# Kernel tuning notes

Measured on AMD Instinct MI355X. Metric: run time of the kernel, lower is better.

The kernel has to match this reference:

```python
import jax, jax.numpy as jnp
import numpy as np

B, N = 8192, 512
WEIGHT_THRESHOLD = 0.0
EPS = 1e-5


def setup_inputs() -> dict:
    key = jax.random.key(0)
    k1, k2, k3 = jax.random.split(key, 3)
    src_points = jax.random.normal(k1, (B, N, 3), dtype=jnp.float32)
    tgt_points = jax.random.normal(k2, (B, N, 3), dtype=jnp.float32)
    weights = jax.random.uniform(k3, (B, N), dtype=jnp.float32)
    return {"src_points": src_points, "tgt_points": tgt_points, "weights": weights}


def _weighted_procrustes(src, tgt, w):
    # threshold + normalize weights  (B, N)
    w = jnp.where(w < WEIGHT_THRESHOLD, jnp.zeros_like(w), w)
    w = w / (jnp.sum(w, axis=1, keepdims=True) + EPS)
    w3 = w[..., None]                                   # (B, N, 1)
    # weighted centroids (B, 1, 3)
    src_c = jnp.sum(w3 * src, axis=1, keepdims=True)
    tgt_c = jnp.sum(w3 * tgt, axis=1, keepdims=True)
    src0 = src - src_c
    tgt0 = tgt - tgt_c
    # weighted covariance H = src0^T (w * tgt0)  -> (B, 3, 3)
    H = jnp.einsum("bni,bnj->bij", src0, w3 * tgt0)
    U, S, Vh = jnp.linalg.svd(H)
    V = jnp.swapaxes(Vh, -1, -2)
    Ut = jnp.swapaxes(U, -1, -2)
    # reflection correction: diag(1, 1, sign(det(V U^T)))
    det = jnp.linalg.det(jnp.matmul(V, Ut))             # (B,)
    ones = jnp.ones((src.shape[0], 2), dtype=src.dtype)
    d = jnp.concatenate([ones, jnp.sign(det)[:, None]], axis=1)  # (B, 3)
    R = jnp.einsum("bij,bj,bjk->bik", V, d, Ut)         # (B, 3, 3)
    t = tgt_c[:, 0, :] - jnp.einsum("bij,bj->bi", R, src_c[:, 0, :])  # (B, 3)
    return R, t


def reference(src_points, tgt_points, weights):
    return _weighted_procrustes(src_points, tgt_points, weights)
```

## Files before the change

kernel.cpp:

```cpp
#include <hip/hip_runtime.h>

#define NPTS 512
#define BLOCK 256
#define XPS 68

__global__ __launch_bounds__(BLOCK) void wproc_moments(
    const float* __restrict__ src,
    const float* __restrict__ tgt,
    const float* __restrict__ wts,
    float* __restrict__ ws)
{
    const int b = blockIdx.x;
    const int t = threadIdx.x;
    const int wave = t >> 6, lane = t & 63;

    __shared__ float s_s[NPTS * 3];
    __shared__ float s_t[NPTS * 3];
    __shared__ float xp[4][16][XPS];
    __shared__ float red[4][16];

    {
        const float4* sb4 = (const float4*)(src + (size_t)b * (NPTS * 3));
        const float4* tb4 = (const float4*)(tgt + (size_t)b * (NPTS * 3));
        float4* ss4 = (float4*)s_s;
        float4* st4 = (float4*)s_t;
        ss4[t] = sb4[t];
        st4[t] = tb4[t];
        if (t < 128) { ss4[256 + t] = sb4[256 + t]; st4[256 + t] = tb4[256 + t]; }
    }
    const float* wb = wts + (size_t)b * NPTS;
    float wA = wb[t];
    float wB = wb[t + 256];
    __syncthreads();

    float acc[16];
    #pragma unroll
    for (int i = 0; i < 16; ++i) acc[i] = 0.f;

    #pragma unroll
    for (int k = 0; k < 2; ++k) {
        const int p = t + k * 256;
        float w = k ? wB : wA;
        w = (w < 0.f) ? 0.f : w;
        const float sx = s_s[3 * p + 0], sy = s_s[3 * p + 1], sz = s_s[3 * p + 2];
        const float tx = s_t[3 * p + 0], ty = s_t[3 * p + 1], tz = s_t[3 * p + 2];
        acc[0] += w;
        acc[1] += w * sx; acc[2] += w * sy; acc[3] += w * sz;
        acc[4] += w * tx; acc[5] += w * ty; acc[6] += w * tz;
        const float wsx = w * sx, wsy = w * sy, wsz = w * sz;
        acc[7]  += wsx * tx; acc[8]  += wsx * ty; acc[9]  += wsx * tz;
        acc[10] += wsy * tx; acc[11] += wsy * ty; acc[12] += wsy * tz;
        acc[13] += wsz * tx; acc[14] += wsz * ty; acc[15] += wsz * tz;
    }

    #pragma unroll
    for (int m = 0; m < 16; ++m) xp[wave][m][lane] = acc[m];
    __syncthreads();

    {
        const int m = lane & 15, q = lane >> 4;
        const float4* row = (const float4*)&xp[wave][m][0] + 4 * q;
        float4 a0 = row[0], a1 = row[1], a2 = row[2], a3 = row[3];
        a0.x += a1.x; a0.y += a1.y; a0.z += a1.z; a0.w += a1.w;
        a2.x += a3.x; a2.y += a3.y; a2.z += a3.z; a2.w += a3.w;
        a0.x += a2.x; a0.y += a2.y; a0.z += a2.z; a0.w += a2.w;
        float v = (a0.x + a0.y) + (a0.z + a0.w);
        v += __shfl_xor(v, 16, 64);
        v += __shfl_xor(v, 32, 64);
        if (q == 0) red[wave][m] = v;
    }
    __syncthreads();

    if (t < 16) {
        ws[(size_t)b * 16 + t] =
            (red[0][t] + red[1][t]) + (red[2][t] + red[3][t]);
    }
}

__global__ __launch_bounds__(BLOCK) void wproc_solve(
    const float* __restrict__ ws,
    float* __restrict__ out,
    int B)
{
    const int b = blockIdx.x * BLOCK + threadIdx.x;
    if (b >= B) return;

    double m[16];
    #pragma unroll
    for (int i = 0; i < 16; ++i) m[i] = (double)ws[(size_t)b * 16 + i];

    const double T = m[0] + 1e-5;
    const double f = 2.0 - m[0] / T;
    const double cs[3] = { m[1] / T, m[2] / T, m[3] / T };
    const double ct[3] = { m[4] / T, m[5] / T, m[6] / T };
    double H[3][3];
    for (int i = 0; i < 3; ++i)
        for (int j = 0; j < 3; ++j)
            H[i][j] = m[7 + i * 3 + j] / T - f * cs[i] * ct[j];

    double A[3][3];
    for (int i = 0; i < 3; ++i)
        for (int j = 0; j < 3; ++j)
            A[i][j] = H[0][i] * H[0][j] + H[1][i] * H[1][j] + H[2][i] * H[2][j];

    double V[3][3] = { {1, 0, 0}, {0, 1, 0}, {0, 0, 1} };
    for (int sweep = 0; sweep < 5; ++sweep) {
        for (int pair = 0; pair < 3; ++pair) {
            const int p = (pair == 2) ? 1 : 0;
            const int q = (pair == 0) ? 1 : 2;
            const double apq = A[p][q];
            if (apq == 0.0) continue;
            const double theta = (A[q][q] - A[p][p]) / (2.0 * apq);
            const double tt = ((theta >= 0.0) ? 1.0 : -1.0)
                            / (fabs(theta) + sqrt(theta * theta + 1.0));
            const double c = 1.0 / sqrt(tt * tt + 1.0);
            const double sn = tt * c;
            for (int k = 0; k < 3; ++k) {
                const double akp = A[k][p], akq = A[k][q];
                A[k][p] = c * akp - sn * akq;
                A[k][q] = sn * akp + c * akq;
            }
            for (int k = 0; k < 3; ++k) {
                const double apk = A[p][k], aqk = A[q][k];
                A[p][k] = c * apk - sn * aqk;
                A[q][k] = sn * apk + c * aqk;
            }
            for (int k = 0; k < 3; ++k) {
                const double vkp = V[k][p], vkq = V[k][q];
                V[k][p] = c * vkp - sn * vkq;
                V[k][q] = sn * vkp + c * vkq;
            }
        }
    }

    const double lam[3] = { A[0][0], A[1][1], A[2][2] };
    int i0 = 0, i1 = 1, i2 = 2;
    if (lam[i0] < lam[i1]) { int tmp = i0; i0 = i1; i1 = tmp; }
    if (lam[i0] < lam[i2]) { int tmp = i0; i0 = i2; i2 = tmp; }
    if (lam[i1] < lam[i2]) { int tmp = i1; i1 = i2; i2 = tmp; }

    const double v1[3] = { V[0][i0], V[1][i0], V[2][i0] };
    const double v2[3] = { V[0][i1], V[1][i1], V[2][i1] };
    const double v3[3] = { v1[1] * v2[2] - v1[2] * v2[1],
                           v1[2] * v2[0] - v1[0] * v2[2],
                           v1[0] * v2[1] - v1[1] * v2[0] };

    double u1[3], u2[3], u3[3];
    for (int i = 0; i < 3; ++i)
        u1[i] = H[i][0] * v1[0] + H[i][1] * v1[1] + H[i][2] * v1[2];
    double n1 = sqrt(u1[0] * u1[0] + u1[1] * u1[1] + u1[2] * u1[2]);
    n1 = (n1 > 1e-30) ? n1 : 1e-30;
    for (int i = 0; i < 3; ++i) u1[i] /= n1;

    for (int i = 0; i < 3; ++i)
        u2[i] = H[i][0] * v2[0] + H[i][1] * v2[1] + H[i][2] * v2[2];
    const double d12 = u1[0] * u2[0] + u1[1] * u2[1] + u1[2] * u2[2];
    for (int i = 0; i < 3; ++i) u2[i] -= d12 * u1[i];
    double n2 = sqrt(u2[0] * u2[0] + u2[1] * u2[1] + u2[2] * u2[2]);
    n2 = (n2 > 1e-30) ? n2 : 1e-30;
    for (int i = 0; i < 3; ++i) u2[i] /= n2;

    u3[0] = u1[1] * u2[2] - u1[2] * u2[1];
    u3[1] = u1[2] * u2[0] - u1[0] * u2[2];
    u3[2] = u1[0] * u2[1] - u1[1] * u2[0];

    double R[3][3];
    for (int i = 0; i < 3; ++i)
        for (int j = 0; j < 3; ++j)
            R[i][j] = v1[i] * u1[j] + v2[i] * u2[j] + v3[i] * u3[j];

    double tv[3];
    for (int i = 0; i < 3; ++i)
        tv[i] = ct[i] - (R[i][0] * cs[0] + R[i][1] * cs[1] + R[i][2] * cs[2]);

    float* outR = out + (size_t)b * 9;
    for (int i = 0; i < 3; ++i)
        for (int j = 0; j < 3; ++j)
            outR[i * 3 + j] = (float)R[i][j];
    float* outT = out + (size_t)B * 9 + (size_t)b * 3;
    for (int i = 0; i < 3; ++i) outT[i] = (float)tv[i];
}

extern "C" void kernel_launch(void* const* d_in, const int* in_sizes, int n_in,
                              void* d_out, int out_size, void* d_ws, size_t ws_size,
                              hipStream_t stream) {
    const float* src = (const float*)d_in[0];
    const float* tgt = (const float*)d_in[1];
    const float* wts = (const float*)d_in[2];
    float* out = (float*)d_out;
    float* ws = (float*)d_ws;
    const int B = out_size / 12;

    wproc_moments<<<B, BLOCK, 0, stream>>>(src, tgt, wts, ws);
    wproc_solve<<<(B + BLOCK - 1) / BLOCK, BLOCK, 0, stream>>>(ws, out, B);
}
```

Before: 146.3 us.

## Assign one wavefront per batch and read points directly from global

The moments kernel now gives each batch item to a single 64-lane wavefront, so one block covers four batches. The shared-memory staging of source and target points and the block-wide barriers are removed. Each lane loads its strided points straight from global memory with stride-3 scalar loads, and the per-wave result goes directly to the workspace. This cuts block count and synchronization, but it trades coalesced float4 loads for uncoalesced scalar loads. It also relies on B being divisible by 4 and uses shared memory written and read within a wave without a barrier.

```diff
diff --git a/kernel.cpp b/kernel.cpp
--- a/kernel.cpp
+++ b/kernel.cpp
@@ -10,40 +10,25 @@
     const float* __restrict__ wts,
     float* __restrict__ ws)
 {
-    const int b = blockIdx.x;
-    const int t = threadIdx.x;
-    const int wave = t >> 6, lane = t & 63;
+    const int wave = threadIdx.x >> 6;
+    const int lane = threadIdx.x & 63;
+    const int b = blockIdx.x * 4 + wave;
 
-    __shared__ float s_s[NPTS * 3];
-    __shared__ float s_t[NPTS * 3];
-    __shared__ float xp[4][16][XPS];
-    __shared__ float red[4][16];
-
-    {
-        const float4* sb4 = (const float4*)(src + (size_t)b * (NPTS * 3));
-        const float4* tb4 = (const float4*)(tgt + (size_t)b * (NPTS * 3));
-        float4* ss4 = (float4*)s_s;
-        float4* st4 = (float4*)s_t;
-        ss4[t] = sb4[t];
-        st4[t] = tb4[t];
-        if (t < 128) { ss4[256 + t] = sb4[256 + t]; st4[256 + t] = tb4[256 + t]; }
-    }
+    const float* sb = src + (size_t)b * (NPTS * 3);
+    const float* tb = tgt + (size_t)b * (NPTS * 3);
     const float* wb = wts + (size_t)b * NPTS;
-    float wA = wb[t];
-    float wB = wb[t + 256];
-    __syncthreads();
 
     float acc[16];
     #pragma unroll
     for (int i = 0; i < 16; ++i) acc[i] = 0.f;
 
     #pragma unroll
-    for (int k = 0; k < 2; ++k) {
-        const int p = t + k * 256;
-        float w = k ? wB : wA;
+    for (int k = 0; k < 8; ++k) {
+        const int p = lane + 64 * k;
+        float w = wb[p];
         w = (w < 0.f) ? 0.f : w;
-        const float sx = s_s[3 * p + 0], sy = s_s[3 * p + 1], sz = s_s[3 * p + 2];
-        const float tx = s_t[3 * p + 0], ty = s_t[3 * p + 1], tz = s_t[3 * p + 2];
+        const float sx = sb[3 * p + 0], sy = sb[3 * p + 1], sz = sb[3 * p + 2];
+        const float tx = tb[3 * p + 0], ty = tb[3 * p + 1], tz = tb[3 * p + 2];
         acc[0] += w;
         acc[1] += w * sx; acc[2] += w * sy; acc[3] += w * sz;
         acc[4] += w * tx; acc[5] += w * ty; acc[6] += w * tz;
@@ -53,9 +38,9 @@
         acc[13] += wsz * tx; acc[14] += wsz * ty; acc[15] += wsz * tz;
     }
 
+    __shared__ float xp[4][16][XPS];
     #pragma unroll
     for (int m = 0; m < 16; ++m) xp[wave][m][lane] = acc[m];
-    __syncthreads();
 
     {
         const int m = lane & 15, q = lane >> 4;
@@ -67,13 +52,7 @@
         float v = (a0.x + a0.y) + (a0.z + a0.w);
         v += __shfl_xor(v, 16, 64);
         v += __shfl_xor(v, 32, 64);
-        if (q == 0) red[wave][m] = v;
-    }
-    __syncthreads();
-
-    if (t < 16) {
-        ws[(size_t)b * 16 + t] =
-            (red[0][t] + red[1][t]) + (red[2][t] + red[3][t]);
+        if (q == 0) ws[(size_t)b * 16 + m] = v;
     }
 }
 
@@ -191,6 +170,6 @@
     float* ws = (float*)d_ws;
     const int B = out_size / 12;
 
-    wproc_moments<<<B, BLOCK, 0, stream>>>(src, tgt, wts, ws);
+    wproc_moments<<<B / 4, BLOCK, 0, stream>>>(src, tgt, wts, ws);
     wproc_solve<<<(B + BLOCK - 1) / BLOCK, BLOCK, 0, stream>>>(ws, out, B);
 }
```

Result: no change. 148.1 us (+1.2%).

## Load point clouds straight into LDS and alias scratch buffers

Applied to the files above, without the earlier changes.

The register-staged copy of src, tgt and weights into shared memory is replaced by `__builtin_amdgcn_global_load_lds` 16-byte direct global-to-LDS transfers, spread across the four waves in 1 KB chunks. The weights are now read from LDS instead of registers. The point buffers and the cross-lane reduction scratch share one aliased shared-memory region, which roughly halves LDS use per block and should allow more resident blocks. A barrier is added before the scratch is overwritten, and the barrier after it is dropped because each wave only reads its own slice, which relies on wave-synchronous LDS ordering.

```diff
diff --git a/kernel.cpp b/kernel.cpp
--- a/kernel.cpp
+++ b/kernel.cpp
@@ -3,6 +3,9 @@
 #define NPTS 512
 #define BLOCK 256
 #define XPS 68
+
+#define GLOBAL_AS(p) ((const __attribute__((address_space(1))) void*)(p))
+#define LDS_AS(p)    ((__attribute__((address_space(3))) void*)(p))
 
 __global__ __launch_bounds__(BLOCK) void wproc_moments(
     const float* __restrict__ src,
@@ -14,24 +17,28 @@
     const int t = threadIdx.x;
     const int wave = t >> 6, lane = t & 63;
 
-    __shared__ float s_s[NPTS * 3];
-    __shared__ float s_t[NPTS * 3];
-    __shared__ float xp[4][16][XPS];
+    __shared__ __align__(16) char smem[4 * 16 * XPS * 4];
     __shared__ float red[4][16];
 
-    {
-        const float4* sb4 = (const float4*)(src + (size_t)b * (NPTS * 3));
-        const float4* tb4 = (const float4*)(tgt + (size_t)b * (NPTS * 3));
-        float4* ss4 = (float4*)s_s;
-        float4* st4 = (float4*)s_t;
-        ss4[t] = sb4[t];
-        st4[t] = tb4[t];
-        if (t < 128) { ss4[256 + t] = sb4[256 + t]; st4[256 + t] = tb4[256 + t]; }
-    }
-    const float* wb = wts + (size_t)b * NPTS;
-    float wA = wb[t];
-    float wB = wb[t + 256];
+    const char* sb = (const char*)(src + (size_t)b * (NPTS * 3));
+    const char* tb = (const char*)(tgt + (size_t)b * (NPTS * 3));
+    const char* wb = (const char*)(wts + (size_t)b * NPTS);
+
+    for (int c = wave; c < 14; c += 4) {
+        const char* g;
+        if (c < 6)       g = sb + (size_t)c * 1024;
+        else if (c < 12) g = tb + (size_t)(c - 6) * 1024;
+        else             g = wb + (size_t)(c - 12) * 1024;
+        __builtin_amdgcn_global_load_lds(
+            GLOBAL_AS(g + lane * 16),
+            LDS_AS(smem + c * 1024),
+            16, 0, 0);
+    }
     __syncthreads();
+
+    const float* s_s = (const float*)smem;
+    const float* s_t = (const float*)(smem + 6144);
+    const float* s_w = (const float*)(smem + 12288);
 
     float acc[16];
     #pragma unroll
@@ -40,7 +47,7 @@
     #pragma unroll
     for (int k = 0; k < 2; ++k) {
         const int p = t + k * 256;
-        float w = k ? wB : wA;
+        float w = s_w[p];
         w = (w < 0.f) ? 0.f : w;
         const float sx = s_s[3 * p + 0], sy = s_s[3 * p + 1], sz = s_s[3 * p + 2];
         const float tx = s_t[3 * p + 0], ty = s_t[3 * p + 1], tz = s_t[3 * p + 2];
@@ -52,10 +59,11 @@
         acc[10] += wsy * tx; acc[11] += wsy * ty; acc[12] += wsy * tz;
         acc[13] += wsz * tx; acc[14] += wsz * ty; acc[15] += wsz * tz;
     }
-
+    __syncthreads();
+
+    float (*xp)[16][XPS] = (float (*)[16][XPS])smem;
     #pragma unroll
     for (int m = 0; m < 16; ++m) xp[wave][m][lane] = acc[m];
-    __syncthreads();
 
     {
         const int m = lane & 15, q = lane >> 4;
```

After: 144.8 us. About the same (-1.1%).
